# Performance work log

Hardware: AMD Instinct MI355X
Metric: run time of the kernel (lower is better)

Reference implementation:

```python
import jax, jax.numpy as jnp
import numpy as np

N_CLASSES = 64  # number of initial (labeled) classes


def _compute_logits_radii(h, protos, radii):
    """Complex-valued radii logits.
    h: [B,N,2,D] (real/imag), protos: [B,2,C,D], radii: [B,C].
    dist[b,n,c] = sum_d (hr-pr)^2 + (hi-pi)^2 (matches _compute_distances_complex).
    logits = -dist / (2*radii)  (standard IMP radii-logit form).
    Expanded as |h|^2 + |p|^2 - 2 h.p so the cross term is a GEMM (no [N,C,D] tensor).
    """
    hr, hi = h[:, :, 0, :], h[:, :, 1, :]          # [B,N,D]
    pr, pi = protos[:, 0], protos[:, 1]            # [B,C,D]
    h_sq = jnp.sum(hr * hr + hi * hi, axis=-1)     # [B,N]
    p_sq = jnp.sum(pr * pr + pi * pi, axis=-1)     # [B,C]
    cross = jnp.einsum('bnd,bcd->bnc', hr, pr) + jnp.einsum('bnd,bcd->bnc', hi, pi)
    dist = h_sq[:, :, None] + p_sq[:, None, :] - 2.0 * cross   # [B,N,C]
    return -dist / (2.0 * radii[:, None, :])


def setup_inputs() -> dict:
    key = jax.random.key(0)
    k1, k2, k3, k4, k5 = jax.random.split(key, 5)
    B, N, C, D = 1, 8192, 512, 512
    h = jax.random.normal(k1, (B, N, 2, D), dtype=jnp.float32)
    protos = jax.random.normal(k2, (B, 2, C, D), dtype=jnp.float32)
    # radii must be positive (it divides the distance); keep away from 0
    radii = jax.random.uniform(k3, (B, C), dtype=jnp.float32) * 0.9 + 0.1
    y = jax.random.randint(k4, (N,), 0, N_CLASSES)
    support_labels = jax.random.randint(k5, (C,), 0, N_CLASSES)
    return {"h": h, "protos": protos, "radii": radii, "y": y,
            "support_labels": support_labels, "n_initial_clusters": N_CLASSES}


def reference(h, protos, radii, y, support_labels, n_initial_clusters):
    logits = _compute_logits_radii(h, protos, radii)[0]          # [N,C], B=1 squeeze
    labels = jnp.where(y >= n_initial_clusters, -1, y)           # [N]
    support_targets = labels[:, None] == support_labels[None, :]  # [N,C] bool

    neg_inf = jnp.asarray(-jnp.inf, logits.dtype)
    # best prototype among the query's own class ('or' target)
    target_logits = jnp.where(support_targets, logits, neg_inf)
    best_targets = jnp.argmax(target_logits, axis=1)             # [N]

    # vectorized per-class best prototype: weights[n,c]=1 iff c is the argmax
    # of logits[n,:] restricted to clusters whose label == support_labels[c]
    max_per_class = jax.ops.segment_max(logits.T, support_labels,
                                        num_segments=N_CLASSES)  # [K,N]
    weights = (logits == max_per_class[support_labels, :].T).astype(logits.dtype)  # [N,C]

    # weighted cross entropy at the 'or' target
    log_probs = jax.nn.log_softmax(logits, axis=1)
    nll = -jnp.take_along_axis(log_probs, best_targets[:, None], axis=1)[:, 0]
    w = jnp.take_along_axis(weights, best_targets[:, None], axis=1)[:, 0]
    loss = jnp.mean(nll * w)

    # accuracy: predicted cluster -> its class label
    support_preds = jnp.argmax(logits, axis=1)
    y_pred = support_labels[support_preds]
    acc_val = jnp.sum((y_pred == labels).astype(jnp.float32))
    return loss, acc_val
```

## Files before the change

kernel.cpp:

```cpp
#include <hip/hip_runtime.h>
#include <hip/hip_bf16.h>
#include <stdint.h>

typedef unsigned short u16;
typedef __attribute__((ext_vector_type(8))) short shortx8;
typedef __attribute__((ext_vector_type(4))) float floatx4;

#define N_ROWS 8192
#define N_COLS 512
#define KDIM   1024

__device__ __forceinline__ u16 f2bf(float f) {
    union { float f; uint32_t u; } x; x.f = f;
    uint32_t u = x.u;
    uint32_t r = (u + 0x7FFFu + ((u >> 16) & 1u)) >> 16;
    return (u16)r;
}

__device__ __forceinline__ u16 f2bf_hw(float f) {
    union { __hip_bfloat16 b; u16 u; } x;
    x.b = __float2bfloat16(f);
    return x.u;
}

__device__ __forceinline__ void async_copy16(const void* g, void* l) {
    __builtin_amdgcn_global_load_lds(
        (const __attribute__((address_space(1))) void*)g,
        (__attribute__((address_space(3))) void*)l, 16, 0, 0);
}

__global__ __launch_bounds__(256) void prep(const float* __restrict__ protos,
                                            u16* __restrict__ bb,
                                            float* __restrict__ psq,
                                            float* __restrict__ out) {
    int t = threadIdx.x, lane = t & 63, w = t >> 6;
    if (blockIdx.x == 0 && t == 0) { out[0] = 0.0f; out[1] = 0.0f; }
    int c = blockIdx.x * 4 + w;
    const float4* pr = (const float4*)(protos + (size_t)c * 512);
    const float4* pi = (const float4*)(protos + 512 * 512 + (size_t)c * 512);
    ushort4* dr = (ushort4*)(bb + (size_t)c * KDIM);
    ushort4* di = (ushort4*)(bb + (size_t)c * KDIM + 512);
    float s = 0.0f;
    #pragma unroll
    for (int j = 0; j < 2; j++) {
        float4 a = pr[lane + j * 64];
        float4 b = pi[lane + j * 64];
        s += a.x * a.x + a.y * a.y + a.z * a.z + a.w * a.w;
        s += b.x * b.x + b.y * b.y + b.z * b.z + b.w * b.w;
        dr[lane + j * 64] = make_ushort4(f2bf(a.x), f2bf(a.y), f2bf(a.z), f2bf(a.w));
        di[lane + j * 64] = make_ushort4(f2bf(b.x), f2bf(b.y), f2bf(b.z), f2bf(b.w));
    }
    #pragma unroll
    for (int off = 32; off; off >>= 1) s += __shfl_xor(s, off);
    if (lane == 0) psq[c] = s;
}

__global__ __launch_bounds__(256) void gemm_fused(const float* __restrict__ h,
                                                  const u16* __restrict__ bb,
                                                  const float* __restrict__ psq,
                                                  const float* __restrict__ radii,
                                                  const int* __restrict__ y,
                                                  const int* __restrict__ slab,
                                                  const int* __restrict__ ninit_p,
                                                  float* __restrict__ pmax_g,
                                                  int* __restrict__ pidx_g,
                                                  float* __restrict__ prmax_g,
                                                  float* __restrict__ pc0_g,
                                                  float* __restrict__ psum_g,
                                                  float* __restrict__ l0arr) {
    constexpr int BM = 128, BN = 64, BK = 64, NSTEP = KDIM / BK;
    __shared__ __align__(16) u16 As[BM * BK];
    __shared__ __align__(16) u16 Bs[2][BN * BK];
    __shared__ float shsq[BM];
    __shared__ float smax[2][128];
    __shared__ int   scol[2][128];
    __shared__ float srmx[2][128];
    __shared__ float sc0v[2][128];
    __shared__ float ssum[2][128];

    int t = threadIdx.x, lane = t & 63, w = t >> 6;
    int wr = (w & 1) * 64;
    int wc = (w >> 1) * 32;

    int bid = blockIdx.x;
    int xcd = bid & 7;
    int idin = bid >> 3;
    int bx = (xcd << 3) | (idin >> 3);
    int by = idin & 7;
    int bm0 = bx * BM;
    int bn0 = by * BN;

    int arow = t >> 1, ahalf = t & 1;
    const float4* gA = (const float4*)(h + (size_t)(bm0 + arow) * KDIM + ahalf * 32);
    u16* lAw[4];
    #pragma unroll
    for (int j = 0; j < 4; j++) {
        int kcg = ahalf * 4 + j;
        lAw[j] = &As[arow * BK + ((kcg ^ (arow & 7)) * 8)];
    }

    int tr = t >> 3, tc = t & 7;
    const u16* gB[2];
    int lBoff[2];
    #pragma unroll
    for (int i = 0; i < 2; i++) {
        int row = tr + 32 * i;
        int kc = tc ^ (row & 7);
        gB[i] = bb + (size_t)(bn0 + row) * KDIM + kc * 8;
        lBoff[i] = (t + 256 * i) * 8;
    }

    floatx4 acc[4][2] = {};
    int kq = lane >> 4, l7 = lane & 7, m = lane & 15;
    int swz0 = ((kq) ^ l7) * 8;
    int swz1 = ((4 + kq) ^ l7) * 8;
    const u16* paA = &As[(wr + m) * BK];

    float hs = 0.0f;
    float4 av[8];

    #pragma unroll
    for (int j = 0; j < 8; j++) av[j] = gA[j];
    #pragma unroll
    for (int i = 0; i < 2; i++) async_copy16(gB[i], &Bs[0][lBoff[i]]);

    for (int step = 0; step < NSTEP; ++step) {
        __syncthreads();
        #pragma unroll
        for (int j = 0; j < 4; j++) {
            float4 a = av[2 * j], b = av[2 * j + 1];
            hs += a.x * a.x + a.y * a.y + a.z * a.z + a.w * a.w
                + b.x * b.x + b.y * b.y + b.z * b.z + b.w * b.w;
            shortx8 p;
            p[0] = (short)f2bf_hw(a.x); p[1] = (short)f2bf_hw(a.y);
            p[2] = (short)f2bf_hw(a.z); p[3] = (short)f2bf_hw(a.w);
            p[4] = (short)f2bf_hw(b.x); p[5] = (short)f2bf_hw(b.y);
            p[6] = (short)f2bf_hw(b.z); p[7] = (short)f2bf_hw(b.w);
            *(shortx8*)lAw[j] = p;
        }
        __syncthreads();
        if (step + 1 < NSTEP) {
            const float4* gAn = gA + (step + 1) * 16;
            #pragma unroll
            for (int j = 0; j < 8; j++) av[j] = gAn[j];
            #pragma unroll
            for (int i = 0; i < 2; i++)
                async_copy16(gB[i] + (size_t)(step + 1) * BK, &Bs[(step + 1) & 1][lBoff[i]]);
        }
        const u16* paB = &Bs[step & 1][(wc + m) * BK];
        #pragma unroll
        for (int s = 0; s < 2; s++) {
            int sw = s ? swz1 : swz0;
            shortx8 af[4], bf[2];
            #pragma unroll
            for (int i = 0; i < 4; i++) af[i] = *(const shortx8*)(paA + i * 16 * BK + sw);
            #pragma unroll
            for (int jj = 0; jj < 2; jj++) bf[jj] = *(const shortx8*)(paB + jj * 16 * BK + sw);
            #pragma unroll
            for (int i = 0; i < 4; i++)
                #pragma unroll
                for (int jj = 0; jj < 2; jj++)
                    acc[i][jj] = __builtin_amdgcn_mfma_f32_16x16x32_bf16(af[i], bf[jj], acc[i][jj], 0, 0, 0);
        }
    }

    hs += __shfl_xor(hs, 1);
    if (ahalf == 0) shsq[arow] = hs;
    __syncthreads();

    int c0 = bn0 + wc + m, c1 = c0 + 16;
    float ps0 = psq[c0], ps1 = psq[c1];
    float inv0 = 0.5f / radii[c0], inv1 = 0.5f / radii[c1];
    int sl0 = slab[c0], sl1 = slab[c1];
    int slabz = slab[0];
    int ninit = ninit_p[0];
    int ch = w >> 1;
    bool isL0 = (bn0 == 0) && (wc == 0) && (m == 0);

    #pragma unroll
    for (int i = 0; i < 4; i++) {
        #pragma unroll
        for (int r = 0; r < 4; r++) {
            int lr = wr + i * 16 + kq * 4 + r;
            int n = bm0 + lr;
            float hsqn = shsq[lr];
            int yv = y[n];
            int lab = (yv >= ninit) ? -1 : yv;
            float v0 = (2.0f * acc[i][0][r] - hsqn - ps0) * inv0;
            float v1 = (2.0f * acc[i][1][r] - hsqn - ps1) * inv1;
            if (isL0) l0arr[n] = v0;

            float bmax = v0; int bcol = c0;
            if (v1 > bmax) { bmax = v1; bcol = c1; }
            float brm = -INFINITY;
            if (sl0 == lab) brm = v0;
            if (sl1 == lab && v1 > brm) brm = v1;
            float bc0 = -INFINITY;
            if (sl0 == slabz) bc0 = v0;
            if (sl1 == slabz && v1 > bc0) bc0 = v1;
            #pragma unroll
            for (int off = 1; off < 16; off <<= 1) {
                float ov = __shfl_xor(bmax, off); int oc = __shfl_xor(bcol, off);
                if (ov > bmax || (ov == bmax && oc < bcol)) { bmax = ov; bcol = oc; }
                float orv = __shfl_xor(brm, off); if (orv > brm) brm = orv;
                float oc0 = __shfl_xor(bc0, off); if (oc0 > bc0) bc0 = oc0;
            }
            float se = __expf(v0 - bmax) + __expf(v1 - bmax);
            #pragma unroll
            for (int off = 1; off < 16; off <<= 1) se += __shfl_xor(se, off);
            if (m == 0) {
                int rl = (w & 1) * 64 + i * 16 + kq * 4 + r;
                smax[ch][rl] = bmax; scol[ch][rl] = bcol;
                srmx[ch][rl] = brm;  sc0v[ch][rl] = bc0; ssum[ch][rl] = se;
            }
        }
    }
    __syncthreads();
    if (t < 128) {
        int n = bm0 + t;
        size_t gi_ = (size_t)by * N_ROWS + n;
        float m0 = smax[0][t], m1 = smax[1][t];
        int i0 = scol[0][t], i1 = scol[1][t];
        float gm; int gi;
        if (m0 > m1 || (m0 == m1 && i0 < i1)) { gm = m0; gi = i0; }
        else { gm = m1; gi = i1; }
        pmax_g[gi_] = gm;
        pidx_g[gi_] = gi;
        prmax_g[gi_] = fmaxf(srmx[0][t], srmx[1][t]);
        pc0_g[gi_]  = fmaxf(sc0v[0][t], sc0v[1][t]);
        psum_g[gi_] = ssum[0][t] * __expf(m0 - gm) + ssum[1][t] * __expf(m1 - gm);
    }
}

__global__ __launch_bounds__(256) void combine(const float* __restrict__ pmax_g,
                                               const int* __restrict__ pidx_g,
                                               const float* __restrict__ prmax_g,
                                               const float* __restrict__ pc0_g,
                                               const float* __restrict__ psum_g,
                                               const float* __restrict__ l0arr,
                                               const int* __restrict__ y,
                                               const int* __restrict__ slab,
                                               const int* __restrict__ ninit_p,
                                               float* __restrict__ out) {
    int t = threadIdx.x, lane = t & 63, w = t >> 6;
    int n = blockIdx.x * 256 + t;

    float gm = -INFINITY; int gi = 0x7fffffff;
    float rm = -INFINITY, c0m = -INFINITY;
    float pm[8];
    #pragma unroll
    for (int cb = 0; cb < 8; cb++) {
        size_t idx = (size_t)cb * N_ROWS + n;
        float p = pmax_g[idx]; int pi = pidx_g[idx];
        pm[cb] = p;
        if (p > gm || (p == gm && pi < gi)) { gm = p; gi = pi; }
        rm = fmaxf(rm, prmax_g[idx]);
        c0m = fmaxf(c0m, pc0_g[idx]);
    }
    float den = 0.0f;
    #pragma unroll
    for (int cb = 0; cb < 8; cb++)
        den += psum_g[(size_t)cb * N_ROWS + n] * __expf(pm[cb] - gm);
    float lse = gm + __logf(den);

    int yv = y[n];
    int lab = (yv >= ninit_p[0]) ? -1 : yv;
    float nll, wgt;
    if (rm != -INFINITY) { nll = lse - rm; wgt = 1.0f; }
    else {
        float l0 = l0arr[n];
        nll = lse - l0;
        wgt = (l0 == c0m) ? 1.0f : 0.0f;
    }
    int ypred = slab[gi];
    float li = nll * wgt * (1.0f / (float)N_ROWS);
    float ai = (ypred == lab) ? 1.0f : 0.0f;

    #pragma unroll
    for (int off = 32; off; off >>= 1) {
        li += __shfl_xor(li, off);
        ai += __shfl_xor(ai, off);
    }
    __shared__ float pl[4], pa_[4];
    if (lane == 0) { pl[w] = li; pa_[w] = ai; }
    __syncthreads();
    if (t == 0) {
        atomicAdd(&out[0], pl[0] + pl[1] + pl[2] + pl[3]);
        atomicAdd(&out[1], pa_[0] + pa_[1] + pa_[2] + pa_[3]);
    }
}

extern "C" void kernel_launch(void* const* d_in, const int* in_sizes, int n_in,
                              void* d_out, int out_size, void* d_ws, size_t ws_size,
                              hipStream_t stream) {
    const float* h      = (const float*)d_in[0];
    const float* protos = (const float*)d_in[1];
    const float* radii  = (const float*)d_in[2];
    const int*   y      = (const int*)d_in[3];
    const int*   slab   = (const int*)d_in[4];
    const int*   ninit  = (const int*)d_in[5];
    float* out = (float*)d_out;

    char* ws = (char*)d_ws;
    u16*   bb    = (u16*)(ws + 16777216);
    float* pmax  = (float*)(ws + 17860608);
    int*   pidx  = (int*)  (ws + 18122752);
    float* prmax = (float*)(ws + 18384896);
    float* pc0   = (float*)(ws + 18647040);
    float* psum  = (float*)(ws + 18909184);
    float* l0arr = (float*)(ws + 19171328);
    float* psq   = (float*)(ws + 17858560);

    prep<<<128, 256, 0, stream>>>(protos, bb, psq, out);
    gemm_fused<<<512, 256, 0, stream>>>(h, bb, psq, radii, y, slab, ninit,
                                        pmax, pidx, prmax, pc0, psum, l0arr);
    combine<<<N_ROWS / 256, 256, 0, stream>>>(pmax, pidx, prmax, pc0, psum,
                                              l0arr, y, slab, ninit, out);
}
```

Measured before the change: 140.0 us.

## Coalesce A-tile loads, defer bf16 conversion past MFMA, request two blocks per CU

The fp32 A tile is now loaded with 16 threads spanning one 64-float row segment, so global loads are fully coalesced instead of each thread reading 32 contiguous floats. The bf16 conversion and LDS store of the next A tile move to after the MFMA block, which lets the prefetched loads overlap compute. Row norms become 8 per-thread partial sums reduced by shuffles. __launch_bounds__(256,2) asks for two resident blocks per CU, which may limit registers and cause spills.

```diff
diff --git a/kernel.cpp b/kernel.cpp
--- a/kernel.cpp
+++ b/kernel.cpp
@@ -55,19 +55,19 @@
     if (lane == 0) psq[c] = s;
 }
 
-__global__ __launch_bounds__(256) void gemm_fused(const float* __restrict__ h,
-                                                  const u16* __restrict__ bb,
-                                                  const float* __restrict__ psq,
-                                                  const float* __restrict__ radii,
-                                                  const int* __restrict__ y,
-                                                  const int* __restrict__ slab,
-                                                  const int* __restrict__ ninit_p,
-                                                  float* __restrict__ pmax_g,
-                                                  int* __restrict__ pidx_g,
-                                                  float* __restrict__ prmax_g,
-                                                  float* __restrict__ pc0_g,
-                                                  float* __restrict__ psum_g,
-                                                  float* __restrict__ l0arr) {
+__global__ __launch_bounds__(256, 2) void gemm_fused(const float* __restrict__ h,
+                                                     const u16* __restrict__ bb,
+                                                     const float* __restrict__ psq,
+                                                     const float* __restrict__ radii,
+                                                     const int* __restrict__ y,
+                                                     const int* __restrict__ slab,
+                                                     const int* __restrict__ ninit_p,
+                                                     float* __restrict__ pmax_g,
+                                                     int* __restrict__ pidx_g,
+                                                     float* __restrict__ prmax_g,
+                                                     float* __restrict__ pc0_g,
+                                                     float* __restrict__ psum_g,
+                                                     float* __restrict__ l0arr) {
     constexpr int BM = 128, BN = 64, BK = 64, NSTEP = KDIM / BK;
     __shared__ __align__(16) u16 As[BM * BK];
     __shared__ __align__(16) u16 Bs[2][BN * BK];
@@ -90,14 +90,11 @@
     int bm0 = bx * BM;
     int bn0 = by * BN;
 
-    int arow = t >> 1, ahalf = t & 1;
-    const float4* gA = (const float4*)(h + (size_t)(bm0 + arow) * KDIM + ahalf * 32);
-    u16* lAw[4];
-    #pragma unroll
-    for (int j = 0; j < 4; j++) {
-        int kcg = ahalf * 4 + j;
-        lAw[j] = &As[arow * BK + ((kcg ^ (arow & 7)) * 8)];
-    }
+    int arow4 = t >> 4;
+    int apos  = t & 15;
+    const float* gA0 = h + (size_t)(bm0 + arow4) * KDIM + apos * 4;
+    int swzA = ((apos >> 1) ^ (arow4 & 7));
+    u16* pAsW = &As[arow4 * 64 + swzA * 8 + (apos & 1) * 4];
 
     int tr = t >> 3, tc = t & 7;
     const u16* gB[2];
@@ -116,33 +113,27 @@
     int swz1 = ((4 + kq) ^ l7) * 8;
     const u16* paA = &As[(wr + m) * BK];
 
-    float hs = 0.0f;
+    float hs[8] = {0, 0, 0, 0, 0, 0, 0, 0};
     float4 av[8];
 
     #pragma unroll
-    for (int j = 0; j < 8; j++) av[j] = gA[j];
+    for (int q = 0; q < 8; q++) av[q] = *(const float4*)(gA0 + (size_t)q * 16 * KDIM);
     #pragma unroll
     for (int i = 0; i < 2; i++) async_copy16(gB[i], &Bs[0][lBoff[i]]);
+    #pragma unroll
+    for (int q = 0; q < 8; q++) {
+        float4 v = av[q];
+        hs[q] += v.x * v.x + v.y * v.y + v.z * v.z + v.w * v.w;
+        *(ushort4*)(pAsW + q * 1024) =
+            make_ushort4(f2bf_hw(v.x), f2bf_hw(v.y), f2bf_hw(v.z), f2bf_hw(v.w));
+    }
+    __syncthreads();
 
     for (int step = 0; step < NSTEP; ++step) {
-        __syncthreads();
-        #pragma unroll
-        for (int j = 0; j < 4; j++) {
-            float4 a = av[2 * j], b = av[2 * j + 1];
-            hs += a.x * a.x + a.y * a.y + a.z * a.z + a.w * a.w
-                + b.x * b.x + b.y * b.y + b.z * b.z + b.w * b.w;
-            shortx8 p;
-            p[0] = (short)f2bf_hw(a.x); p[1] = (short)f2bf_hw(a.y);
-            p[2] = (short)f2bf_hw(a.z); p[3] = (short)f2bf_hw(a.w);
-            p[4] = (short)f2bf_hw(b.x); p[5] = (short)f2bf_hw(b.y);
-            p[6] = (short)f2bf_hw(b.z); p[7] = (short)f2bf_hw(b.w);
-            *(shortx8*)lAw[j] = p;
-        }
-        __syncthreads();
         if (step + 1 < NSTEP) {
-            const float4* gAn = gA + (step + 1) * 16;
-            #pragma unroll
-            for (int j = 0; j < 8; j++) av[j] = gAn[j];
+            const float* gAn = gA0 + (step + 1) * 64;
+            #pragma unroll
+            for (int q = 0; q < 8; q++) av[q] = *(const float4*)(gAn + (size_t)q * 16 * KDIM);
             #pragma unroll
             for (int i = 0; i < 2; i++)
                 async_copy16(gB[i] + (size_t)(step + 1) * BK, &Bs[(step + 1) & 1][lBoff[i]]);
@@ -162,10 +153,28 @@
                 for (int jj = 0; jj < 2; jj++)
                     acc[i][jj] = __builtin_amdgcn_mfma_f32_16x16x32_bf16(af[i], bf[jj], acc[i][jj], 0, 0, 0);
         }
-    }
-
-    hs += __shfl_xor(hs, 1);
-    if (ahalf == 0) shsq[arow] = hs;
+        if (step + 1 < NSTEP) {
+            __syncthreads();
+            #pragma unroll
+            for (int q = 0; q < 8; q++) {
+                float4 v = av[q];
+                hs[q] += v.x * v.x + v.y * v.y + v.z * v.z + v.w * v.w;
+                *(ushort4*)(pAsW + q * 1024) =
+                    make_ushort4(f2bf_hw(v.x), f2bf_hw(v.y), f2bf_hw(v.z), f2bf_hw(v.w));
+            }
+            __syncthreads();
+        }
+    }
+
+    #pragma unroll
+    for (int q = 0; q < 8; q++) {
+        float v = hs[q];
+        v += __shfl_xor(v, 1);
+        v += __shfl_xor(v, 2);
+        v += __shfl_xor(v, 4);
+        v += __shfl_xor(v, 8);
+        if ((t & 15) == 0) shsq[q * 16 + arow4] = v;
+    }
     __syncthreads();
 
     int c0 = bn0 + wc + m, c1 = c0 + 16;
@@ -303,13 +312,13 @@
 
     char* ws = (char*)d_ws;
     u16*   bb    = (u16*)(ws + 16777216);
+    float* psq   = (float*)(ws + 17858560);
     float* pmax  = (float*)(ws + 17860608);
     int*   pidx  = (int*)  (ws + 18122752);
     float* prmax = (float*)(ws + 18384896);
     float* pc0   = (float*)(ws + 18647040);
     float* psum  = (float*)(ws + 18909184);
     float* l0arr = (float*)(ws + 19171328);
-    float* psq   = (float*)(ws + 17858560);
 
     prep<<<128, 256, 0, stream>>>(protos, bb, psq, out);
     gemm_fused<<<512, 256, 0, stream>>>(h, bb, psq, radii, y, slab, ninit,
```

Measured after the change: 123.7 us. 1.13x faster.

## Fuse GEMM and combine with full-row tiles covering all prototypes per block

Applied to the files above, without the earlier changes.

Each block now owns 32 rows and all 512 prototype columns (8 waves of 64 columns), so the row-wise max, logsumexp and label reductions finish inside the block. This removes the partial-result buffers and the separate combine kernel. B fragments are read straight from global/L2 into registers instead of being staged through LDS, and the A tile is double-buffered in LDS with a single barrier per step. The cost is only 256 blocks with little A reuse per B load, which leans heavily on L2 bandwidth for the prototype matrix.

```diff
diff --git a/kernel.cpp b/kernel.cpp
--- a/kernel.cpp
+++ b/kernel.cpp
@@ -15,18 +15,6 @@
     uint32_t u = x.u;
     uint32_t r = (u + 0x7FFFu + ((u >> 16) & 1u)) >> 16;
     return (u16)r;
-}
-
-__device__ __forceinline__ u16 f2bf_hw(float f) {
-    union { __hip_bfloat16 b; u16 u; } x;
-    x.b = __float2bfloat16(f);
-    return x.u;
-}
-
-__device__ __forceinline__ void async_copy16(const void* g, void* l) {
-    __builtin_amdgcn_global_load_lds(
-        (const __attribute__((address_space(1))) void*)g,
-        (__attribute__((address_space(3))) void*)l, 16, 0, 0);
 }
 
 __global__ __launch_bounds__(256) void prep(const float* __restrict__ protos,
@@ -55,149 +43,136 @@
     if (lane == 0) psq[c] = s;
 }
 
-__global__ __launch_bounds__(256) void gemm_fused(const float* __restrict__ h,
-                                                  const u16* __restrict__ bb,
-                                                  const float* __restrict__ psq,
-                                                  const float* __restrict__ radii,
-                                                  const int* __restrict__ y,
-                                                  const int* __restrict__ slab,
-                                                  const int* __restrict__ ninit_p,
-                                                  float* __restrict__ pmax_g,
-                                                  int* __restrict__ pidx_g,
-                                                  float* __restrict__ prmax_g,
-                                                  float* __restrict__ pc0_g,
-                                                  float* __restrict__ psum_g,
-                                                  float* __restrict__ l0arr) {
-    constexpr int BM = 128, BN = 64, BK = 64, NSTEP = KDIM / BK;
-    __shared__ __align__(16) u16 As[BM * BK];
-    __shared__ __align__(16) u16 Bs[2][BN * BK];
-    __shared__ float shsq[BM];
-    __shared__ float smax[2][128];
-    __shared__ int   scol[2][128];
-    __shared__ float srmx[2][128];
-    __shared__ float sc0v[2][128];
-    __shared__ float ssum[2][128];
+__global__ __launch_bounds__(512, 2) void gemm_full(const float* __restrict__ h,
+                                                    const u16* __restrict__ bb,
+                                                    const float* __restrict__ psq,
+                                                    const float* __restrict__ radii,
+                                                    const int* __restrict__ y,
+                                                    const int* __restrict__ slab,
+                                                    const int* __restrict__ ninit_p,
+                                                    float* __restrict__ out) {
+    constexpr int BK = 64, NSTEP = KDIM / BK;
+    __shared__ __align__(16) u16 As[2][32 * BK];
+    __shared__ float shsq[32];
+    __shared__ float wmax[8][32];
+    __shared__ int   wcol[8][32];
+    __shared__ float wrm_[8][32];
+    __shared__ float wc0_[8][32];
+    __shared__ float wse_[8][32];
+    __shared__ float sl0_[32];
 
     int t = threadIdx.x, lane = t & 63, w = t >> 6;
-    int wr = (w & 1) * 64;
-    int wc = (w >> 1) * 32;
-
-    int bid = blockIdx.x;
-    int xcd = bid & 7;
-    int idin = bid >> 3;
-    int bx = (xcd << 3) | (idin >> 3);
-    int by = idin & 7;
-    int bm0 = bx * BM;
-    int bn0 = by * BN;
-
-    int arow = t >> 1, ahalf = t & 1;
-    const float4* gA = (const float4*)(h + (size_t)(bm0 + arow) * KDIM + ahalf * 32);
-    u16* lAw[4];
+    int bm0 = blockIdx.x * 32;
+
+    int arow = t >> 4;
+    int ac4  = t & 15;
+    const float4* gA = (const float4*)(h + (size_t)(bm0 + arow) * KDIM) + ac4;
+    int aoff = arow * BK + ((ac4 >> 1) ^ (arow & 7)) * 8 + (ac4 & 1) * 4;
+    u16* asw[2] = { &As[0][aoff], &As[1][aoff] };
+
+    int kq = lane >> 4, m = lane & 15, l7 = lane & 7;
+    int wc = w * 64;
+    int cols[4];
+    const u16* gB[4];
     #pragma unroll
     for (int j = 0; j < 4; j++) {
-        int kcg = ahalf * 4 + j;
-        lAw[j] = &As[arow * BK + ((kcg ^ (arow & 7)) * 8)];
-    }
-
-    int tr = t >> 3, tc = t & 7;
-    const u16* gB[2];
-    int lBoff[2];
-    #pragma unroll
-    for (int i = 0; i < 2; i++) {
-        int row = tr + 32 * i;
-        int kc = tc ^ (row & 7);
-        gB[i] = bb + (size_t)(bn0 + row) * KDIM + kc * 8;
-        lBoff[i] = (t + 256 * i) * 8;
-    }
-
-    floatx4 acc[4][2] = {};
-    int kq = lane >> 4, l7 = lane & 7, m = lane & 15;
-    int swz0 = ((kq) ^ l7) * 8;
-    int swz1 = ((4 + kq) ^ l7) * 8;
-    const u16* paA = &As[(wr + m) * BK];
-
+        cols[j] = wc + 16 * j + m;
+        gB[j] = bb + (size_t)cols[j] * KDIM + kq * 8;
+    }
+    int sw0 = (kq ^ l7) * 8;
+    int sw1 = ((4 + kq) ^ l7) * 8;
+    const u16* paA0 = &As[0][m * BK];
+    const u16* paA1 = &As[1][m * BK];
+
+    floatx4 acc[2][4] = {};
     float hs = 0.0f;
-    float4 av[8];
-
-    #pragma unroll
-    for (int j = 0; j < 8; j++) av[j] = gA[j];
-    #pragma unroll
-    for (int i = 0; i < 2; i++) async_copy16(gB[i], &Bs[0][lBoff[i]]);
+
+    {
+        float4 v = gA[0];
+        hs += v.x * v.x + v.y * v.y + v.z * v.z + v.w * v.w;
+        *(ushort4*)asw[0] = make_ushort4(f2bf(v.x), f2bf(v.y), f2bf(v.z), f2bf(v.w));
+    }
+    __syncthreads();
 
     for (int step = 0; step < NSTEP; ++step) {
+        int cur = step & 1;
+        int k0 = step * BK;
+        float4 av;
+        bool pre = (step + 1 < NSTEP);
+        if (pre) av = gA[(step + 1) * 16];
+
+        shortx8 bf0[4], bf1[4];
+        #pragma unroll
+        for (int j = 0; j < 4; j++) bf0[j] = *(const shortx8*)(gB[j] + k0);
+        #pragma unroll
+        for (int j = 0; j < 4; j++) bf1[j] = *(const shortx8*)(gB[j] + k0 + 32);
+
+        const u16* paA = cur ? paA1 : paA0;
+        shortx8 a00 = *(const shortx8*)(paA + sw0);
+        shortx8 a01 = *(const shortx8*)(paA + 16 * BK + sw0);
+        shortx8 a10 = *(const shortx8*)(paA + sw1);
+        shortx8 a11 = *(const shortx8*)(paA + 16 * BK + sw1);
+
+        #pragma unroll
+        for (int j = 0; j < 4; j++) {
+            acc[0][j] = __builtin_amdgcn_mfma_f32_16x16x32_bf16(a00, bf0[j], acc[0][j], 0, 0, 0);
+            acc[1][j] = __builtin_amdgcn_mfma_f32_16x16x32_bf16(a01, bf0[j], acc[1][j], 0, 0, 0);
+        }
+        #pragma unroll
+        for (int j = 0; j < 4; j++) {
+            acc[0][j] = __builtin_amdgcn_mfma_f32_16x16x32_bf16(a10, bf1[j], acc[0][j], 0, 0, 0);
+            acc[1][j] = __builtin_amdgcn_mfma_f32_16x16x32_bf16(a11, bf1[j], acc[1][j], 0, 0, 0);
+        }
+
+        if (pre) {
+            hs += av.x * av.x + av.y * av.y + av.z * av.z + av.w * av.w;
+            *(ushort4*)asw[cur ^ 1] =
+                make_ushort4(f2bf(av.x), f2bf(av.y), f2bf(av.z), f2bf(av.w));
+        }
         __syncthreads();
-        #pragma unroll
-        for (int j = 0; j < 4; j++) {
-            float4 a = av[2 * j], b = av[2 * j + 1];
-            hs += a.x * a.x + a.y * a.y + a.z * a.z + a.w * a.w
-                + b.x * b.x + b.y * b.y + b.z * b.z + b.w * b.w;
-            shortx8 p;
-            p[0] = (short)f2bf_hw(a.x); p[1] = (short)f2bf_hw(a.y);
-            p[2] = (short)f2bf_hw(a.z); p[3] = (short)f2bf_hw(a.w);
-            p[4] = (short)f2bf_hw(b.x); p[5] = (short)f2bf_hw(b.y);
-            p[6] = (short)f2bf_hw(b.z); p[7] = (short)f2bf_hw(b.w);
-            *(shortx8*)lAw[j] = p;
-        }
-        __syncthreads();
-        if (step + 1 < NSTEP) {
-            const float4* gAn = gA + (step + 1) * 16;
-            #pragma unroll
-            for (int j = 0; j < 8; j++) av[j] = gAn[j];
-            #pragma unroll
-            for (int i = 0; i < 2; i++)
-                async_copy16(gB[i] + (size_t)(step + 1) * BK, &Bs[(step + 1) & 1][lBoff[i]]);
-        }
-        const u16* paB = &Bs[step & 1][(wc + m) * BK];
-        #pragma unroll
-        for (int s = 0; s < 2; s++) {
-            int sw = s ? swz1 : swz0;
-            shortx8 af[4], bf[2];
-            #pragma unroll
-            for (int i = 0; i < 4; i++) af[i] = *(const shortx8*)(paA + i * 16 * BK + sw);
-            #pragma unroll
-            for (int jj = 0; jj < 2; jj++) bf[jj] = *(const shortx8*)(paB + jj * 16 * BK + sw);
-            #pragma unroll
-            for (int i = 0; i < 4; i++)
-                #pragma unroll
-                for (int jj = 0; jj < 2; jj++)
-                    acc[i][jj] = __builtin_amdgcn_mfma_f32_16x16x32_bf16(af[i], bf[jj], acc[i][jj], 0, 0, 0);
-        }
     }
 
     hs += __shfl_xor(hs, 1);
-    if (ahalf == 0) shsq[arow] = hs;
+    hs += __shfl_xor(hs, 2);
+    hs += __shfl_xor(hs, 4);
+    hs += __shfl_xor(hs, 8);
+    if (ac4 == 0) shsq[arow] = hs;
     __syncthreads();
 
-    int c0 = bn0 + wc + m, c1 = c0 + 16;
-    float ps0 = psq[c0], ps1 = psq[c1];
-    float inv0 = 0.5f / radii[c0], inv1 = 0.5f / radii[c1];
-    int sl0 = slab[c0], sl1 = slab[c1];
+    float psqv[4], invv[4]; int slv[4];
+    #pragma unroll
+    for (int j = 0; j < 4; j++) {
+        psqv[j] = psq[cols[j]];
+        invv[j] = 0.5f / radii[cols[j]];
+        slv[j]  = slab[cols[j]];
+    }
     int slabz = slab[0];
     int ninit = ninit_p[0];
-    int ch = w >> 1;
-    bool isL0 = (bn0 == 0) && (wc == 0) && (m == 0);
-
-    #pragma unroll
-    for (int i = 0; i < 4; i++) {
+
+    #pragma unroll
+    for (int i = 0; i < 2; i++) {
         #pragma unroll
         for (int r = 0; r < 4; r++) {
-            int lr = wr + i * 16 + kq * 4 + r;
-            int n = bm0 + lr;
+            int lr = i * 16 + kq * 4 + r;
             float hsqn = shsq[lr];
-            int yv = y[n];
+            int yv = y[bm0 + lr];
             int lab = (yv >= ninit) ? -1 : yv;
-            float v0 = (2.0f * acc[i][0][r] - hsqn - ps0) * inv0;
-            float v1 = (2.0f * acc[i][1][r] - hsqn - ps1) * inv1;
-            if (isL0) l0arr[n] = v0;
-
-            float bmax = v0; int bcol = c0;
-            if (v1 > bmax) { bmax = v1; bcol = c1; }
-            float brm = -INFINITY;
-            if (sl0 == lab) brm = v0;
-            if (sl1 == lab && v1 > brm) brm = v1;
-            float bc0 = -INFINITY;
-            if (sl0 == slabz) bc0 = v0;
-            if (sl1 == slabz && v1 > bc0) bc0 = v1;
+            float v[4];
+            #pragma unroll
+            for (int j = 0; j < 4; j++)
+                v[j] = (2.0f * acc[i][j][r] - hsqn - psqv[j]) * invv[j];
+            if (w == 0 && m == 0) sl0_[lr] = v[0];
+
+            float bmax = v[0]; int bcol = cols[0];
+            #pragma unroll
+            for (int j = 1; j < 4; j++)
+                if (v[j] > bmax) { bmax = v[j]; bcol = cols[j]; }
+            float brm = -INFINITY, bc0 = -INFINITY;
+            #pragma unroll
+            for (int j = 0; j < 4; j++) {
+                if (slv[j] == lab   && v[j] > brm) brm = v[j];
+                if (slv[j] == slabz && v[j] > bc0) bc0 = v[j];
+            }
             #pragma unroll
             for (int off = 1; off < 16; off <<= 1) {
                 float ov = __shfl_xor(bmax, off); int oc = __shfl_xor(bcol, off);
@@ -205,88 +180,58 @@
                 float orv = __shfl_xor(brm, off); if (orv > brm) brm = orv;
                 float oc0 = __shfl_xor(bc0, off); if (oc0 > bc0) bc0 = oc0;
             }
-            float se = __expf(v0 - bmax) + __expf(v1 - bmax);
+            float se = __expf(v[0] - bmax) + __expf(v[1] - bmax)
+                     + __expf(v[2] - bmax) + __expf(v[3] - bmax);
             #pragma unroll
             for (int off = 1; off < 16; off <<= 1) se += __shfl_xor(se, off);
             if (m == 0) {
-                int rl = (w & 1) * 64 + i * 16 + kq * 4 + r;
-                smax[ch][rl] = bmax; scol[ch][rl] = bcol;
-                srmx[ch][rl] = brm;  sc0v[ch][rl] = bc0; ssum[ch][rl] = se;
+                wmax[w][lr] = bmax; wcol[w][lr] = bcol;
+                wrm_[w][lr] = brm;  wc0_[w][lr] = bc0; wse_[w][lr] = se;
             }
         }
     }
     __syncthreads();
-    if (t < 128) {
+
+    if (t < 32) {
         int n = bm0 + t;
-        size_t gi_ = (size_t)by * N_ROWS + n;
-        float m0 = smax[0][t], m1 = smax[1][t];
-        int i0 = scol[0][t], i1 = scol[1][t];
-        float gm; int gi;
-        if (m0 > m1 || (m0 == m1 && i0 < i1)) { gm = m0; gi = i0; }
-        else { gm = m1; gi = i1; }
-        pmax_g[gi_] = gm;
-        pidx_g[gi_] = gi;
-        prmax_g[gi_] = fmaxf(srmx[0][t], srmx[1][t]);
-        pc0_g[gi_]  = fmaxf(sc0v[0][t], sc0v[1][t]);
-        psum_g[gi_] = ssum[0][t] * __expf(m0 - gm) + ssum[1][t] * __expf(m1 - gm);
-    }
-}
-
-__global__ __launch_bounds__(256) void combine(const float* __restrict__ pmax_g,
-                                               const int* __restrict__ pidx_g,
-                                               const float* __restrict__ prmax_g,
-                                               const float* __restrict__ pc0_g,
-                                               const float* __restrict__ psum_g,
-                                               const float* __restrict__ l0arr,
-                                               const int* __restrict__ y,
-                                               const int* __restrict__ slab,
-                                               const int* __restrict__ ninit_p,
-                                               float* __restrict__ out) {
-    int t = threadIdx.x, lane = t & 63, w = t >> 6;
-    int n = blockIdx.x * 256 + t;
-
-    float gm = -INFINITY; int gi = 0x7fffffff;
-    float rm = -INFINITY, c0m = -INFINITY;
-    float pm[8];
-    #pragma unroll
-    for (int cb = 0; cb < 8; cb++) {
-        size_t idx = (size_t)cb * N_ROWS + n;
-        float p = pmax_g[idx]; int pi = pidx_g[idx];
-        pm[cb] = p;
-        if (p > gm || (p == gm && pi < gi)) { gm = p; gi = pi; }
-        rm = fmaxf(rm, prmax_g[idx]);
-        c0m = fmaxf(c0m, pc0_g[idx]);
-    }
-    float den = 0.0f;
-    #pragma unroll
-    for (int cb = 0; cb < 8; cb++)
-        den += psum_g[(size_t)cb * N_ROWS + n] * __expf(pm[cb] - gm);
-    float lse = gm + __logf(den);
-
-    int yv = y[n];
-    int lab = (yv >= ninit_p[0]) ? -1 : yv;
-    float nll, wgt;
-    if (rm != -INFINITY) { nll = lse - rm; wgt = 1.0f; }
-    else {
-        float l0 = l0arr[n];
-        nll = lse - l0;
-        wgt = (l0 == c0m) ? 1.0f : 0.0f;
-    }
-    int ypred = slab[gi];
-    float li = nll * wgt * (1.0f / (float)N_ROWS);
-    float ai = (ypred == lab) ? 1.0f : 0.0f;
-
-    #pragma unroll
-    for (int off = 32; off; off >>= 1) {
-        li += __shfl_xor(li, off);
-        ai += __shfl_xor(ai, off);
-    }
-    __shared__ float pl[4], pa_[4];
-    if (lane == 0) { pl[w] = li; pa_[w] = ai; }
-    __syncthreads();
-    if (t == 0) {
-        atomicAdd(&out[0], pl[0] + pl[1] + pl[2] + pl[3]);
-        atomicAdd(&out[1], pa_[0] + pa_[1] + pa_[2] + pa_[3]);
+        float gm = -INFINITY; int gi = 0x7fffffff;
+        float rm = -INFINITY, c0m = -INFINITY;
+        float wm[8];
+        #pragma unroll
+        for (int w2 = 0; w2 < 8; w2++) {
+            float p = wmax[w2][t]; int pi = wcol[w2][t];
+            wm[w2] = p;
+            if (p > gm || (p == gm && pi < gi)) { gm = p; gi = pi; }
+            float orv = wrm_[w2][t]; if (orv > rm) rm = orv;
+            float oc0 = wc0_[w2][t]; if (oc0 > c0m) c0m = oc0;
+        }
+        float den = 0.0f;
+        #pragma unroll
+        for (int w2 = 0; w2 < 8; w2++)
+            den += wse_[w2][t] * __expf(wm[w2] - gm);
+        float lse = gm + __logf(den);
+
+        int yv = y[n];
+        int lab = (yv >= ninit) ? -1 : yv;
+        float nll, wgt;
+        if (rm != -INFINITY) { nll = lse - rm; wgt = 1.0f; }
+        else {
+            float l0 = sl0_[t];
+            nll = lse - l0;
+            wgt = (l0 == c0m) ? 1.0f : 0.0f;
+        }
+        int ypred = slab[gi];
+        float li = nll * wgt * (1.0f / (float)N_ROWS);
+        float ai = (ypred == lab) ? 1.0f : 0.0f;
+        #pragma unroll
+        for (int off = 16; off; off >>= 1) {
+            li += __shfl_xor(li, off);
+            ai += __shfl_xor(ai, off);
+        }
+        if (t == 0) {
+            atomicAdd(&out[0], li);
+            atomicAdd(&out[1], ai);
+        }
     }
 }
 
@@ -302,18 +247,9 @@
     float* out = (float*)d_out;
 
     char* ws = (char*)d_ws;
-    u16*   bb    = (u16*)(ws + 16777216);
-    float* pmax  = (float*)(ws + 17860608);
-    int*   pidx  = (int*)  (ws + 18122752);
-    float* prmax = (float*)(ws + 18384896);
-    float* pc0   = (float*)(ws + 18647040);
-    float* psum  = (float*)(ws + 18909184);
-    float* l0arr = (float*)(ws + 19171328);
-    float* psq   = (float*)(ws + 17858560);
+    u16*   bb  = (u16*)(ws);
+    float* psq = (float*)(ws + 1048576);
 
     prep<<<128, 256, 0, stream>>>(protos, bb, psq, out);
-    gemm_fused<<<512, 256, 0, stream>>>(h, bb, psq, radii, y, slab, ninit,
-                                        pmax, pidx, prmax, pc0, psum, l0arr);
-    combine<<<N_ROWS / 256, 256, 0, stream>>>(pmax, pidx, prmax, pc0, psum,
-                                              l0arr, y, slab, ninit, out);
-}
+    gemm_full<<<256, 512, 0, stream>>>(h, bb, psq, radii, y, slab, ninit, out);
+}
```

Result: faster. 130.4 us (-6.9%).

## Stream fp32 A tiles directly into LDS and convert to bf16 at fragment load

Applied to the files above, without the earlier changes.

Activation tiles are now copied from global memory straight into LDS as fp32 with async global-to-LDS loads, instead of passing through registers, being converted to bf16 and stored. The bf16 conversion and the |h|^2 accumulation move to the point where MFMA fragments are read, using a packed v_cvt_pk_bf16_f32 instruction. The double buffer for B is removed, so loads for each step are issued and waited on inside the same iteration, with no prefetch overlap. Row norms are then reduced across lanes with shuffles, and the workspace layout is compacted.

```diff
diff --git a/kernel.cpp b/kernel.cpp
--- a/kernel.cpp
+++ b/kernel.cpp
@@ -1,5 +1,4 @@
 #include <hip/hip_runtime.h>
-#include <hip/hip_bf16.h>
 #include <stdint.h>
 
 typedef unsigned short u16;
@@ -17,16 +16,16 @@
     return (u16)r;
 }
 
-__device__ __forceinline__ u16 f2bf_hw(float f) {
-    union { __hip_bfloat16 b; u16 u; } x;
-    x.b = __float2bfloat16(f);
-    return x.u;
-}
-
 __device__ __forceinline__ void async_copy16(const void* g, void* l) {
     __builtin_amdgcn_global_load_lds(
         (const __attribute__((address_space(1))) void*)g,
         (__attribute__((address_space(3))) void*)l, 16, 0, 0);
+}
+
+__device__ __forceinline__ uint32_t cvt_pk_bf16(float lo, float hi) {
+    uint32_t r;
+    asm("v_cvt_pk_bf16_f32 %0, %1, %2" : "=v"(r) : "v"(lo), "v"(hi));
+    return r;
 }
 
 __global__ __launch_bounds__(256) void prep(const float* __restrict__ protos,
@@ -69,8 +68,8 @@
                                                   float* __restrict__ psum_g,
                                                   float* __restrict__ l0arr) {
     constexpr int BM = 128, BN = 64, BK = 64, NSTEP = KDIM / BK;
-    __shared__ __align__(16) u16 As[BM * BK];
-    __shared__ __align__(16) u16 Bs[2][BN * BK];
+    __shared__ __align__(16) float Asf[BM * BK];
+    __shared__ __align__(16) u16 Bs[BN * BK];
     __shared__ float shsq[BM];
     __shared__ float smax[2][128];
     __shared__ int   scol[2][128];
@@ -90,18 +89,13 @@
     int bm0 = bx * BM;
     int bn0 = by * BN;
 
-    int arow = t >> 1, ahalf = t & 1;
-    const float4* gA = (const float4*)(h + (size_t)(bm0 + arow) * KDIM + ahalf * 32);
-    u16* lAw[4];
-    #pragma unroll
-    for (int j = 0; j < 4; j++) {
-        int kcg = ahalf * 4 + j;
-        lAw[j] = &As[arow * BK + ((kcg ^ (arow & 7)) * 8)];
-    }
+    int arow0 = t >> 4;
+    int cg = (t & 15) ^ arow0;
+    const float* gA = h + (size_t)(bm0 + arow0) * KDIM + cg * 4;
+    float* lA = &Asf[t * 4];
 
     int tr = t >> 3, tc = t & 7;
-    const u16* gB[2];
-    int lBoff[2];
+    const u16* gB[2]; int lBoff[2];
     #pragma unroll
     for (int i = 0; i < 2; i++) {
         int row = tr + 32 * i;
@@ -111,51 +105,42 @@
     }
 
     floatx4 acc[4][2] = {};
+    float hs[4] = {0.0f, 0.0f, 0.0f, 0.0f};
     int kq = lane >> 4, l7 = lane & 7, m = lane & 15;
-    int swz0 = ((kq) ^ l7) * 8;
-    int swz1 = ((4 + kq) ^ l7) * 8;
-    const u16* paA = &As[(wr + m) * BK];
-
-    float hs = 0.0f;
-    float4 av[8];
-
-    #pragma unroll
-    for (int j = 0; j < 8; j++) av[j] = gA[j];
-    #pragma unroll
-    for (int i = 0; i < 2; i++) async_copy16(gB[i], &Bs[0][lBoff[i]]);
+    const u16* paB = &Bs[(wc + m) * BK];
 
     for (int step = 0; step < NSTEP; ++step) {
         __syncthreads();
         #pragma unroll
-        for (int j = 0; j < 4; j++) {
-            float4 a = av[2 * j], b = av[2 * j + 1];
-            hs += a.x * a.x + a.y * a.y + a.z * a.z + a.w * a.w
-                + b.x * b.x + b.y * b.y + b.z * b.z + b.w * b.w;
-            shortx8 p;
-            p[0] = (short)f2bf_hw(a.x); p[1] = (short)f2bf_hw(a.y);
-            p[2] = (short)f2bf_hw(a.z); p[3] = (short)f2bf_hw(a.w);
-            p[4] = (short)f2bf_hw(b.x); p[5] = (short)f2bf_hw(b.y);
-            p[6] = (short)f2bf_hw(b.z); p[7] = (short)f2bf_hw(b.w);
-            *(shortx8*)lAw[j] = p;
-        }
+        for (int i = 0; i < 8; i++)
+            async_copy16(gA + (size_t)i * 16 * KDIM + step * BK, lA + i * 1024);
+        #pragma unroll
+        for (int i = 0; i < 2; i++)
+            async_copy16(gB[i] + step * BK, &Bs[lBoff[i]]);
         __syncthreads();
-        if (step + 1 < NSTEP) {
-            const float4* gAn = gA + (step + 1) * 16;
-            #pragma unroll
-            for (int j = 0; j < 8; j++) av[j] = gAn[j];
-            #pragma unroll
-            for (int i = 0; i < 2; i++)
-                async_copy16(gB[i] + (size_t)(step + 1) * BK, &Bs[(step + 1) & 1][lBoff[i]]);
-        }
-        const u16* paB = &Bs[step & 1][(wc + m) * BK];
+
         #pragma unroll
         for (int s = 0; s < 2; s++) {
-            int sw = s ? swz1 : swz0;
+            int g = s * 4 + kq;
             shortx8 af[4], bf[2];
             #pragma unroll
-            for (int i = 0; i < 4; i++) af[i] = *(const shortx8*)(paA + i * 16 * BK + sw);
-            #pragma unroll
-            for (int jj = 0; jj < 2; jj++) bf[jj] = *(const shortx8*)(paB + jj * 16 * BK + sw);
+            for (int i = 0; i < 4; i++) {
+                const float* rowp = &Asf[(wr + i * 16 + m) * BK];
+                float4 fa = *(const float4*)(rowp + (((2 * g)     ^ m) * 4));
+                float4 fb = *(const float4*)(rowp + (((2 * g + 1) ^ m) * 4));
+                hs[i] += fa.x * fa.x + fa.y * fa.y + fa.z * fa.z + fa.w * fa.w
+                       + fb.x * fb.x + fb.y * fb.y + fb.z * fb.z + fb.w * fb.w;
+                union { shortx8 v; uint32_t u[4]; } pk;
+                pk.u[0] = cvt_pk_bf16(fa.x, fa.y);
+                pk.u[1] = cvt_pk_bf16(fa.z, fa.w);
+                pk.u[2] = cvt_pk_bf16(fb.x, fb.y);
+                pk.u[3] = cvt_pk_bf16(fb.z, fb.w);
+                af[i] = pk.v;
+            }
+            int sw = (g ^ l7) * 8;
+            #pragma unroll
+            for (int jj = 0; jj < 2; jj++)
+                bf[jj] = *(const shortx8*)(paB + jj * 16 * BK + sw);
             #pragma unroll
             for (int i = 0; i < 4; i++)
                 #pragma unroll
@@ -164,8 +149,13 @@
         }
     }
 
-    hs += __shfl_xor(hs, 1);
-    if (ahalf == 0) shsq[arow] = hs;
+    #pragma unroll
+    for (int i = 0; i < 4; i++) {
+        float v = hs[i];
+        v += __shfl_xor(v, 16);
+        v += __shfl_xor(v, 32);
+        if (w < 2 && kq == 0) shsq[wr + i * 16 + m] = v;
+    }
     __syncthreads();
 
     int c0 = bn0 + wc + m, c1 = c0 + 16;
@@ -302,14 +292,14 @@
     float* out = (float*)d_out;
 
     char* ws = (char*)d_ws;
-    u16*   bb    = (u16*)(ws + 16777216);
-    float* pmax  = (float*)(ws + 17860608);
-    int*   pidx  = (int*)  (ws + 18122752);
-    float* prmax = (float*)(ws + 18384896);
-    float* pc0   = (float*)(ws + 18647040);
-    float* psum  = (float*)(ws + 18909184);
-    float* l0arr = (float*)(ws + 19171328);
-    float* psq   = (float*)(ws + 17858560);
+    u16*   bb    = (u16*)(ws);
+    float* psq   = (float*)(ws + 1048576);
+    float* pmax  = (float*)(ws + 1050624);
+    int*   pidx  = (int*)  (ws + 1312768);
+    float* prmax = (float*)(ws + 1574912);
+    float* pc0   = (float*)(ws + 1837056);
+    float* psum  = (float*)(ws + 2099200);
+    float* l0arr = (float*)(ws + 2361344);
 
     prep<<<128, 256, 0, stream>>>(protos, bb, psq, out);
     gemm_fused<<<512, 256, 0, stream>>>(h, bb, psq, radii, y, slab, ninit,
```

Result: faster. 120.5 us (-13.9%).
